# Performance work log

Hardware: AMD Instinct MI355X
Metric: run time of the kernel (lower is better)

Reference implementation:

```python
import jax, jax.numpy as jnp
import numpy as np

NUM_ANCHORS = 5
NUM_CLASSES = 20


def setup_inputs() -> dict:
    key = jax.random.key(0)
    k1, k2, k3, k4 = jax.random.split(key, 4)
    N, H, W, M = 64, 52, 52, 32
    img = 1664
    x = jax.random.normal(k1, (N, NUM_ANCHORS * (5 + NUM_CLASSES), H, W), jnp.float32)
    anchors = jnp.array([[1.08, 1.19], [3.42, 4.41], [6.63, 11.38],
                         [9.42, 5.11], [16.62, 10.52]], jnp.float32)
    # valid gt boxes in xyxy pixel coords
    xy = jax.random.uniform(k2, (N, M, 2), jnp.float32) * (img * 0.8)
    wh = jax.random.uniform(k3, (N, M, 2), jnp.float32) * (img * 0.2) + 1.0
    gt_boxes = jnp.concatenate([xy, xy + wh], axis=-1)
    gt_labels = jax.random.randint(k4, (N, M), 0, NUM_CLASSES)
    return dict(x=x, anchors=anchors, gt_boxes=gt_boxes, gt_labels=gt_labels,
                img_h=img, img_w=img)


def _format_outputs(x, anchors, img_h, img_w):
    # x: [N, A*(5+C), H, W] -> (coords [N,HW,A,4] (x,y,w,h), obj [N,HW,A], scores [N,HW,A,C])
    N, _, H, W = x.shape
    A = anchors.shape[0]
    t = x.reshape(N, A, 5 + NUM_CLASSES, H, W).transpose(0, 3, 4, 1, 2)  # [N,H,W,A,5+C]
    c_x = jnp.arange(W, dtype=x.dtype) * (img_w / W)
    c_y = jnp.arange(H, dtype=x.dtype) * (img_h / H)
    b_x = jax.nn.sigmoid(t[..., 0]) + c_x[None, None, :, None]   # [N,H,W,A]
    b_y = jax.nn.sigmoid(t[..., 1]) + c_y[None, :, None, None]
    b_w = (img_w / W) * anchors[:, 0] * jnp.exp(t[..., 2])
    b_h = (img_h / H) * anchors[:, 1] * jnp.exp(t[..., 3])
    coords = jnp.stack([b_x, b_y, b_w, b_h], axis=-1).reshape(N, H * W, A, 4)
    b_o = jax.nn.sigmoid(t[..., 4]).reshape(N, H * W, A)
    scores = t[..., 5:].reshape(N, H * W, A, NUM_CLASSES)
    return coords, b_o, scores


def reference(x, anchors, gt_boxes, gt_labels, img_h, img_w):
    coords, b_o, scores = _format_outputs(x, anchors, img_h, img_w)
    # pred_boxes[..., 2:] += pred_boxes[..., :2]  (xywh -> xyxy)
    boxes = jnp.concatenate([coords[..., :2], coords[..., :2] + coords[..., 2:]], axis=-1)  # [N,HW,A,4]
    # box_iou: pred [N,HW,A,1,4] vs gt [N,1,1,M,4] -> [N,HW,A,M]
    p = boxes[..., None, :]
    g = gt_boxes[:, None, None, :, :]
    lt = jnp.maximum(p[..., :2], g[..., :2])
    rb = jnp.minimum(p[..., 2:], g[..., 2:])
    whi = jnp.clip(rb - lt, 0.0)
    inter = whi[..., 0] * whi[..., 1]
    area_p = (boxes[..., 2] - boxes[..., 0]) * (boxes[..., 3] - boxes[..., 1])
    area_g = (gt_boxes[..., 2] - gt_boxes[..., 0]) * (gt_boxes[..., 3] - gt_boxes[..., 1])
    iou = inter / (area_p[..., None] + area_g[:, None, None, :] - inter)   # [N,HW,A,M]

    cell_sel = iou.max(axis=(2, 3)) > 0.0                 # [N,HW]
    best_a = jnp.argmax(iou.max(axis=3), axis=2)          # [N,HW] best anchor per cell
    iou_best = jnp.take_along_axis(iou, best_a[..., None, None], axis=2)[:, :, 0, :]  # [N,HW,M]
    max_iou = iou_best.max(axis=-1)                       # [N,HW]
    gt_idx = jnp.argmax(iou_best, axis=-1)                # [N,HW]

    sel_box = jnp.take_along_axis(boxes, best_a[..., None, None], axis=2)[:, :, 0, :]   # [N,HW,4]
    sel_o = jnp.take_along_axis(b_o, best_a[..., None], axis=2)[:, :, 0]                # [N,HW]
    sel_sc = jnp.take_along_axis(scores, best_a[..., None, None], axis=2)[:, :, 0, :]   # [N,HW,C]
    g_box = jnp.take_along_axis(gt_boxes, gt_idx[..., None], axis=1)                    # [N,HW,4]
    g_lab = jnp.take_along_axis(gt_labels, gt_idx, axis=1)                              # [N,HW]

    m = cell_sel.astype(x.dtype)
    objectness_loss = (jnp.sum(m * (sel_o - max_iou) ** 2)
                       + 0.5 * jnp.sum((1.0 - m) * b_o.max(axis=2) ** 2))
    bbox_loss = (jnp.sum(m * jnp.sum((sel_box[..., :2] - g_box[..., :2]) ** 2, axis=-1))
                 + jnp.sum(m * jnp.sum((jnp.sqrt(sel_box[..., 2:]) - jnp.sqrt(g_box[..., 2:])) ** 2, axis=-1)))
    logp = jax.nn.log_softmax(sel_sc, axis=-1)
    ce = -jnp.take_along_axis(logp, g_lab[..., None], axis=-1)[..., 0]
    clf_loss = jnp.sum(m * ce)
    return jnp.stack([objectness_loss, bbox_loss, clf_loss])
```

## Files before the change

kernel.cpp:

```cpp
#include <hip/hip_runtime.h>
#include <math.h>

#define A_ 5
#define C_ 20
#define N_ 64
#define H_ 52
#define W_ 52
#define HW_ (H_ * W_)
#define M_ 32
#define CH_ (A_ * (5 + C_))
#define NBLK_X 11
#define NBLK (NBLK_X * N_)

__device__ __forceinline__ float sigmoidf_(float v) {
    return 1.0f / (1.0f + __expf(-v));
}

__global__ __launch_bounds__(256) void yolo_main_kernel(
    const float* __restrict__ x,
    const float* __restrict__ anchors,
    const float* __restrict__ gt,
    const int* __restrict__ glab,
    const void* img_h_p, const void* img_w_p,
    float* __restrict__ ws)
{
    __shared__ float s_g[M_][4];
    __shared__ float s_area[M_];
    __shared__ int   s_lab[M_];
    __shared__ float s_anch[A_ * 2];
    __shared__ float s_red[4][3];

    const int n = blockIdx.y;
    const int tid = threadIdx.x;
    const int cell = blockIdx.x * 256 + tid;

    if (tid < M_) {
        float g0 = gt[((size_t)n * M_ + tid) * 4 + 0];
        float g1 = gt[((size_t)n * M_ + tid) * 4 + 1];
        float g2 = gt[((size_t)n * M_ + tid) * 4 + 2];
        float g3 = gt[((size_t)n * M_ + tid) * 4 + 3];
        s_g[tid][0] = g0; s_g[tid][1] = g1;
        s_g[tid][2] = g2; s_g[tid][3] = g3;
        s_area[tid] = (g2 - g0) * (g3 - g1);
        s_lab[tid] = glab[n * M_ + tid];
    } else if (tid >= 64 && tid < 64 + A_ * 2) {
        s_anch[tid - 64] = anchors[tid - 64];
    }
    __syncthreads();

    int ibw = *(const int*)img_w_p;
    float img_w = (ibw > 0 && ibw < 1000000) ? (float)ibw : *(const float*)img_w_p;
    int ibh = *(const int*)img_h_p;
    float img_h = (ibh > 0 && ibh < 1000000) ? (float)ibh : *(const float*)img_h_p;
    const float sx = img_w / (float)W_;
    const float sy = img_h / (float)H_;

    float obj_s = 0.0f, bbox_s = 0.0f, clf_s = 0.0f;

    if (cell < HW_) {
        const int wi = cell % W_;
        const int hi = cell / W_;
        const float cx = (float)wi * sx;
        const float cy = (float)hi * sy;

        float best_i = 0.0f, best_u = 1.0f;
        int   best_a = 0, best_m = 0;
        float sxl = 0.f, syl = 0.f, sxr = 0.f, syr = 0.f, so = 0.f;
        float bomax = -1e30f;

        const size_t nbase = (size_t)n * CH_ * HW_ + (size_t)cell;

        #pragma unroll
        for (int a = 0; a < A_; ++a) {
            const float* p = x + nbase + (size_t)a * 25 * HW_;
            float t0 = p[0];
            float t1 = p[HW_];
            float t2 = p[2 * (size_t)HW_];
            float t3 = p[3 * (size_t)HW_];
            float t4 = p[4 * (size_t)HW_];

            float bxv = sigmoidf_(t0) + cx;
            float byv = sigmoidf_(t1) + cy;
            float bw  = sx * s_anch[2 * a]     * __expf(t2);
            float bh  = sy * s_anch[2 * a + 1] * __expf(t3);
            float x1 = bxv, y1 = byv, x2 = bxv + bw, y2 = byv + bh;
            float ap = (x2 - x1) * (y2 - y1);
            float ov = sigmoidf_(t4);
            bomax = fmaxf(bomax, ov);

            float ai = 0.0f, au = 1.0f;
            int   am = 0;
            #pragma unroll 8
            for (int m = 0; m < M_; ++m) {
                float wxi = fminf(x2, s_g[m][2]) - fmaxf(x1, s_g[m][0]);
                float hyi = fminf(y2, s_g[m][3]) - fmaxf(y1, s_g[m][1]);
                wxi = fmaxf(wxi, 0.0f);
                hyi = fmaxf(hyi, 0.0f);
                float inter = wxi * hyi;
                float uni = ap + s_area[m] - inter;
                if (inter * au > ai * uni) { ai = inter; au = uni; am = m; }
            }
            bool upd = (a == 0) || (ai * best_u > best_i * au);
            if (upd) {
                best_i = ai; best_u = au; best_a = a; best_m = am;
                sxl = x1; syl = y1; sxr = x2; syr = y2; so = ov;
            }
        }

        const bool selc = best_i > 0.0f;
        const float miou = best_i / best_u;

        if (selc) {
            float d = so - miou;
            obj_s = d * d;

            const float* g = s_g[best_m];
            float d0 = sxl - g[0];
            float d1 = syl - g[1];
            float d2 = sqrtf(sxr) - sqrtf(g[2]);
            float d3 = sqrtf(syr) - sqrtf(g[3]);
            bbox_s = d0 * d0 + d1 * d1 + d2 * d2 + d3 * d3;

            const float* ps = x + nbase + (size_t)(best_a * 25 + 5) * HW_;
            float sc[C_];
            float mx = -1e30f;
            #pragma unroll
            for (int j = 0; j < C_; ++j) {
                sc[j] = ps[(size_t)j * HW_];
                mx = fmaxf(mx, sc[j]);
            }
            float se = 0.0f;
            #pragma unroll
            for (int j = 0; j < C_; ++j) se += __expf(sc[j] - mx);
            const int lab = s_lab[best_m];
            float scl = sc[0];
            #pragma unroll
            for (int j = 1; j < C_; ++j) scl = (j == lab) ? sc[j] : scl;
            clf_s = mx + __logf(se) - scl;
        } else {
            obj_s = 0.5f * bomax * bomax;
        }
    }

    #pragma unroll
    for (int off = 32; off > 0; off >>= 1) {
        obj_s  += __shfl_down(obj_s,  off, 64);
        bbox_s += __shfl_down(bbox_s, off, 64);
        clf_s  += __shfl_down(clf_s,  off, 64);
    }
    const int wid = tid >> 6;
    if ((tid & 63) == 0) {
        s_red[wid][0] = obj_s;
        s_red[wid][1] = bbox_s;
        s_red[wid][2] = clf_s;
    }
    __syncthreads();
    if (tid == 0) {
        float o = 0.f, b = 0.f, c = 0.f;
        #pragma unroll
        for (int w = 0; w < 4; ++w) {
            o += s_red[w][0]; b += s_red[w][1]; c += s_red[w][2];
        }
        const int bid = blockIdx.y * gridDim.x + blockIdx.x;
        ws[bid * 3 + 0] = o;
        ws[bid * 3 + 1] = b;
        ws[bid * 3 + 2] = c;
    }
}

__global__ __launch_bounds__(256) void yolo_reduce_kernel(
    const float* __restrict__ ws, float* __restrict__ out)
{
    __shared__ float s_red[4][3];
    const int tid = threadIdx.x;
    float o = 0.f, b = 0.f, c = 0.f;
    for (int e = tid; e < NBLK; e += 256) {
        o += ws[e * 3 + 0];
        b += ws[e * 3 + 1];
        c += ws[e * 3 + 2];
    }
    #pragma unroll
    for (int off = 32; off > 0; off >>= 1) {
        o += __shfl_down(o, off, 64);
        b += __shfl_down(b, off, 64);
        c += __shfl_down(c, off, 64);
    }
    const int wid = tid >> 6;
    if ((tid & 63) == 0) {
        s_red[wid][0] = o; s_red[wid][1] = b; s_red[wid][2] = c;
    }
    __syncthreads();
    if (tid == 0) {
        float oo = 0.f, bb = 0.f, cc = 0.f;
        #pragma unroll
        for (int w = 0; w < 4; ++w) {
            oo += s_red[w][0]; bb += s_red[w][1]; cc += s_red[w][2];
        }
        out[0] = oo; out[1] = bb; out[2] = cc;
    }
}

extern "C" void kernel_launch(void* const* d_in, const int* in_sizes, int n_in,
                              void* d_out, int out_size, void* d_ws, size_t ws_size,
                              hipStream_t stream) {
    const float* x    = (const float*)d_in[0];
    const float* anch = (const float*)d_in[1];
    const float* gt   = (const float*)d_in[2];
    const int*   gl   = (const int*)d_in[3];
    const void*  ih   = d_in[4];
    const void*  iw   = d_in[5];
    float* out = (float*)d_out;
    float* ws  = (float*)d_ws;

    dim3 grid(NBLK_X, N_);
    yolo_main_kernel<<<grid, dim3(256), 0, stream>>>(x, anch, gt, gl, ih, iw, ws);
    yolo_reduce_kernel<<<1, 256, 0, stream>>>(ws, out);
}
```

Measured before the change: 145.0 us.

## Spread anchors across wavefronts and combine per-cell results through shared memory

Each block now covers 64 cells with 5 wavefronts, one per anchor. Each thread computes the IoU scan for a single anchor, and the first wavefront picks the best anchor per cell from shared memory before computing the losses. This gives 5x more threads and more memory-level parallelism than the old one-thread-per-cell loop, which ran five serial anchor iterations over 11 blocks per image. In exchange, the loss tail runs on only one of the five wavefronts, a shared-memory exchange and a barrier are added, GT boxes are read from global memory as float4 instead of staged in LDS, and the softmax becomes an online single pass.

Result: no change. 142.6 us (-1.7%).

```diff
diff --git a/kernel.cpp b/kernel.cpp
--- a/kernel.cpp
+++ b/kernel.cpp
@@ -9,14 +9,11 @@
 #define HW_ (H_ * W_)
 #define M_ 32
 #define CH_ (A_ * (5 + C_))
-#define NBLK_X 11
+#define CPB 64
+#define NBLK_X ((HW_ + CPB - 1) / CPB)
 #define NBLK (NBLK_X * N_)
 
-__device__ __forceinline__ float sigmoidf_(float v) {
-    return 1.0f / (1.0f + __expf(-v));
-}
-
-__global__ __launch_bounds__(256) void yolo_main_kernel(
+__global__ __launch_bounds__(320) void yolo_main(
     const float* __restrict__ x,
     const float* __restrict__ anchors,
     const float* __restrict__ gt,
@@ -24,29 +21,14 @@
     const void* img_h_p, const void* img_w_p,
     float* __restrict__ ws)
 {
-    __shared__ float s_g[M_][4];
-    __shared__ float s_area[M_];
-    __shared__ int   s_lab[M_];
-    __shared__ float s_anch[A_ * 2];
-    __shared__ float s_red[4][3];
-
-    const int n = blockIdx.y;
-    const int tid = threadIdx.x;
-    const int cell = blockIdx.x * 256 + tid;
-
-    if (tid < M_) {
-        float g0 = gt[((size_t)n * M_ + tid) * 4 + 0];
-        float g1 = gt[((size_t)n * M_ + tid) * 4 + 1];
-        float g2 = gt[((size_t)n * M_ + tid) * 4 + 2];
-        float g3 = gt[((size_t)n * M_ + tid) * 4 + 3];
-        s_g[tid][0] = g0; s_g[tid][1] = g1;
-        s_g[tid][2] = g2; s_g[tid][3] = g3;
-        s_area[tid] = (g2 - g0) * (g3 - g1);
-        s_lab[tid] = glab[n * M_ + tid];
-    } else if (tid >= 64 && tid < 64 + A_ * 2) {
-        s_anch[tid - 64] = anchors[tid - 64];
-    }
-    __syncthreads();
+    __shared__ float s_c[8][A_][CPB];
+
+    const int tid  = threadIdx.x;
+    const int a    = tid >> 6;
+    const int lane = tid & 63;
+    const int n    = blockIdx.y;
+    const int cell = blockIdx.x * CPB + lane;
+    const bool valid = cell < HW_;
 
     int ibw = *(const int*)img_w_p;
     float img_w = (ibw > 0 && ibw < 1000000) ? (float)ibw : *(const float*)img_w_p;
@@ -55,120 +37,125 @@
     const float sx = img_w / (float)W_;
     const float sy = img_h / (float)H_;
 
-    float obj_s = 0.0f, bbox_s = 0.0f, clf_s = 0.0f;
-
-    if (cell < HW_) {
+    const float ax = anchors[2 * a];
+    const float ay = anchors[2 * a + 1];
+
+    float bi = 0.f, bu = 1.f;
+    int   bm = 0;
+    float x1 = 0.f, y1 = 0.f, x2 = 0.f, y2 = 0.f, ov = 0.f;
+
+    if (valid) {
         const int wi = cell % W_;
         const int hi = cell / W_;
-        const float cx = (float)wi * sx;
-        const float cy = (float)hi * sy;
-
-        float best_i = 0.0f, best_u = 1.0f;
-        int   best_a = 0, best_m = 0;
-        float sxl = 0.f, syl = 0.f, sxr = 0.f, syr = 0.f, so = 0.f;
+        const size_t base = (size_t)n * CH_ * HW_ + (size_t)a * 25 * HW_ + cell;
+        float t0 = x[base];
+        float t1 = x[base + (size_t)HW_];
+        float t2 = x[base + 2 * (size_t)HW_];
+        float t3 = x[base + 3 * (size_t)HW_];
+        float t4 = x[base + 4 * (size_t)HW_];
+
+        float bx = 1.f / (1.f + __expf(-t0)) + (float)wi * sx;
+        float by = 1.f / (1.f + __expf(-t1)) + (float)hi * sy;
+        float bw = sx * ax * __expf(t2);
+        float bh = sy * ay * __expf(t3);
+        x1 = bx; y1 = by; x2 = bx + bw; y2 = by + bh;
+        ov = 1.f / (1.f + __expf(-t4));
+        float ap = (x2 - x1) * (y2 - y1);
+
+        const float4* gtv = (const float4*)(gt + (size_t)n * M_ * 4);
+        #pragma unroll 8
+        for (int m = 0; m < M_; ++m) {
+            float4 g = gtv[m];
+            float area = (g.z - g.x) * (g.w - g.y);
+            float wxi = fminf(x2, g.z) - fmaxf(x1, g.x);
+            float hyi = fminf(y2, g.w) - fmaxf(y1, g.y);
+            wxi = fmaxf(wxi, 0.f);
+            hyi = fmaxf(hyi, 0.f);
+            float inter = wxi * hyi;
+            float uni = ap + area - inter;
+            if (inter * bu > bi * uni) { bi = inter; bu = uni; bm = m; }
+        }
+    }
+
+    s_c[0][a][lane] = bi;
+    s_c[1][a][lane] = bu;
+    s_c[2][a][lane] = x1;
+    s_c[3][a][lane] = y1;
+    s_c[4][a][lane] = x2;
+    s_c[5][a][lane] = y2;
+    s_c[6][a][lane] = ov;
+    s_c[7][a][lane] = __int_as_float(bm);
+    __syncthreads();
+
+    if (tid < 64) {
+        float obj = 0.f, bbx = 0.f, clf = 0.f;
+
+        float Bi = 0.f, Bu = 1.f;
+        int Ba = 0, Bm = 0;
+        float X1 = 0.f, Y1 = 0.f, X2 = 0.f, Y2 = 0.f, O = 0.f;
         float bomax = -1e30f;
-
-        const size_t nbase = (size_t)n * CH_ * HW_ + (size_t)cell;
-
         #pragma unroll
-        for (int a = 0; a < A_; ++a) {
-            const float* p = x + nbase + (size_t)a * 25 * HW_;
-            float t0 = p[0];
-            float t1 = p[HW_];
-            float t2 = p[2 * (size_t)HW_];
-            float t3 = p[3 * (size_t)HW_];
-            float t4 = p[4 * (size_t)HW_];
-
-            float bxv = sigmoidf_(t0) + cx;
-            float byv = sigmoidf_(t1) + cy;
-            float bw  = sx * s_anch[2 * a]     * __expf(t2);
-            float bh  = sy * s_anch[2 * a + 1] * __expf(t3);
-            float x1 = bxv, y1 = byv, x2 = bxv + bw, y2 = byv + bh;
-            float ap = (x2 - x1) * (y2 - y1);
-            float ov = sigmoidf_(t4);
-            bomax = fmaxf(bomax, ov);
-
-            float ai = 0.0f, au = 1.0f;
-            int   am = 0;
-            #pragma unroll 8
-            for (int m = 0; m < M_; ++m) {
-                float wxi = fminf(x2, s_g[m][2]) - fmaxf(x1, s_g[m][0]);
-                float hyi = fminf(y2, s_g[m][3]) - fmaxf(y1, s_g[m][1]);
-                wxi = fmaxf(wxi, 0.0f);
-                hyi = fmaxf(hyi, 0.0f);
-                float inter = wxi * hyi;
-                float uni = ap + s_area[m] - inter;
-                if (inter * au > ai * uni) { ai = inter; au = uni; am = m; }
+        for (int aa = 0; aa < A_; ++aa) {
+            float ci = s_c[0][aa][lane];
+            float cu = s_c[1][aa][lane];
+            float co = s_c[6][aa][lane];
+            bomax = fmaxf(bomax, co);
+            bool upd = (aa == 0) || (ci * Bu > Bi * cu);
+            if (upd) {
+                Bi = ci; Bu = cu; Ba = aa;
+                Bm = __float_as_int(s_c[7][aa][lane]);
+                X1 = s_c[2][aa][lane]; Y1 = s_c[3][aa][lane];
+                X2 = s_c[4][aa][lane]; Y2 = s_c[5][aa][lane];
+                O = co;
             }
-            bool upd = (a == 0) || (ai * best_u > best_i * au);
-            if (upd) {
-                best_i = ai; best_u = au; best_a = a; best_m = am;
-                sxl = x1; syl = y1; sxr = x2; syr = y2; so = ov;
+        }
+
+        if (valid) {
+            if (Bi > 0.f) {
+                float miou = Bi / Bu;
+                float d = O - miou;
+                obj = d * d;
+
+                float4 g = ((const float4*)gt)[n * M_ + Bm];
+                float d0 = X1 - g.x;
+                float d1 = Y1 - g.y;
+                float d2 = sqrtf(X2) - sqrtf(g.z);
+                float d3 = sqrtf(Y2) - sqrtf(g.w);
+                bbx = d0 * d0 + d1 * d1 + d2 * d2 + d3 * d3;
+
+                const size_t sb = (size_t)n * CH_ * HW_ + (size_t)(Ba * 25 + 5) * HW_ + cell;
+                const int lab = glab[n * M_ + Bm];
+                float mx = -1e30f, se = 0.f, scl = 0.f;
+                #pragma unroll
+                for (int j = 0; j < C_; ++j) {
+                    float v = x[sb + (size_t)j * HW_];
+                    float nm = fmaxf(mx, v);
+                    se = se * __expf(mx - nm) + __expf(v - nm);
+                    mx = nm;
+                    scl = (j == lab) ? v : scl;
+                }
+                clf = mx + __logf(se) - scl;
+            } else {
+                obj = 0.5f * bomax * bomax;
             }
         }
 
-        const bool selc = best_i > 0.0f;
-        const float miou = best_i / best_u;
-
-        if (selc) {
-            float d = so - miou;
-            obj_s = d * d;
-
-            const float* g = s_g[best_m];
-            float d0 = sxl - g[0];
-            float d1 = syl - g[1];
-            float d2 = sqrtf(sxr) - sqrtf(g[2]);
-            float d3 = sqrtf(syr) - sqrtf(g[3]);
-            bbox_s = d0 * d0 + d1 * d1 + d2 * d2 + d3 * d3;
-
-            const float* ps = x + nbase + (size_t)(best_a * 25 + 5) * HW_;
-            float sc[C_];
-            float mx = -1e30f;
-            #pragma unroll
-            for (int j = 0; j < C_; ++j) {
-                sc[j] = ps[(size_t)j * HW_];
-                mx = fmaxf(mx, sc[j]);
-            }
-            float se = 0.0f;
-            #pragma unroll
-            for (int j = 0; j < C_; ++j) se += __expf(sc[j] - mx);
-            const int lab = s_lab[best_m];
-            float scl = sc[0];
-            #pragma unroll
-            for (int j = 1; j < C_; ++j) scl = (j == lab) ? sc[j] : scl;
-            clf_s = mx + __logf(se) - scl;
-        } else {
-            obj_s = 0.5f * bomax * bomax;
-        }
-    }
-
-    #pragma unroll
-    for (int off = 32; off > 0; off >>= 1) {
-        obj_s  += __shfl_down(obj_s,  off, 64);
-        bbox_s += __shfl_down(bbox_s, off, 64);
-        clf_s  += __shfl_down(clf_s,  off, 64);
-    }
-    const int wid = tid >> 6;
-    if ((tid & 63) == 0) {
-        s_red[wid][0] = obj_s;
-        s_red[wid][1] = bbox_s;
-        s_red[wid][2] = clf_s;
-    }
-    __syncthreads();
-    if (tid == 0) {
-        float o = 0.f, b = 0.f, c = 0.f;
         #pragma unroll
-        for (int w = 0; w < 4; ++w) {
-            o += s_red[w][0]; b += s_red[w][1]; c += s_red[w][2];
-        }
-        const int bid = blockIdx.y * gridDim.x + blockIdx.x;
-        ws[bid * 3 + 0] = o;
-        ws[bid * 3 + 1] = b;
-        ws[bid * 3 + 2] = c;
+        for (int off = 32; off > 0; off >>= 1) {
+            obj += __shfl_down(obj, off, 64);
+            bbx += __shfl_down(bbx, off, 64);
+            clf += __shfl_down(clf, off, 64);
+        }
+        if (tid == 0) {
+            const int bid = blockIdx.y * gridDim.x + blockIdx.x;
+            ws[bid * 3 + 0] = obj;
+            ws[bid * 3 + 1] = bbx;
+            ws[bid * 3 + 2] = clf;
+        }
     }
 }
 
-__global__ __launch_bounds__(256) void yolo_reduce_kernel(
+__global__ __launch_bounds__(256) void yolo_reduce(
     const float* __restrict__ ws, float* __restrict__ out)
 {
     __shared__ float s_red[4][3];
@@ -213,6 +200,6 @@
     float* ws  = (float*)d_ws;
 
     dim3 grid(NBLK_X, N_);
-    yolo_main_kernel<<<grid, dim3(256), 0, stream>>>(x, anch, gt, gl, ih, iw, ws);
-    yolo_reduce_kernel<<<1, 256, 0, stream>>>(ws, out);
+    yolo_main<<<grid, dim3(320), 0, stream>>>(x, anch, gt, gl, ih, iw, ws);
+    yolo_reduce<<<1, 256, 0, stream>>>(ws, out);
 }
```
